# Performance work log

Measured on AMD Instinct MI355X. Metric: run time of the kernel, lower is better.

Reference implementation:

```python
import jax, jax.numpy as jnp
import numpy as np

N, F, H, E, R = 100000, 256, 64, 800000, 7
EPS = 1e-5

def _layernorm(x, g, b):
    mu = jnp.mean(x, axis=-1, keepdims=True)
    var = jnp.mean((x - mu) ** 2, axis=-1, keepdims=True)
    return (x - mu) * jax.lax.rsqrt(var + EPS) * g + b

def setup_inputs() -> dict:
    key = jax.random.key(0)
    ks = jax.random.split(key, 16)
    block_features = jax.random.normal(ks[0], (N, F), dtype=jnp.float32)
    src = jax.random.randint(ks[1], (E,), 0, N).astype(jnp.float32)
    dst = jax.random.randint(ks[2], (E,), 0, N).astype(jnp.float32)
    rel = jax.random.randint(ks[3], (E,), 0, R).astype(jnp.float32)
    w = jax.random.uniform(ks[4], (E,), dtype=jnp.float32)
    typed_edges = jnp.stack([src, dst, rel, w], axis=1)  # [E,4]
    def lin(k, fan_in, fan_out):
        s = 1.0 / np.sqrt(fan_in)
        k1, k2 = jax.random.split(k)
        return (jax.random.uniform(k1, (fan_in, fan_out), jnp.float32, -s, s),
                jax.random.uniform(k2, (fan_out,), jnp.float32, -s, s))
    W1, b1 = lin(ks[5], F, H)
    W2, b2 = lin(ks[6], H, H)
    rel_emb = jax.random.normal(ks[7], (R, H), dtype=jnp.float32)
    Wm1, bm1 = lin(ks[8], 3 * H + 1, H)
    Wm2, bm2 = lin(ks[9], H, H)
    Wg1, bg1 = lin(ks[10], 2 * H, H)
    Wg2, bg2 = lin(ks[11], H, H)
    return dict(block_features=block_features, typed_edges=typed_edges,
                W1=W1, b1=b1, g1=jnp.ones(H), be1=jnp.zeros(H), W2=W2, b2=b2,
                rel_emb=rel_emb, Wm1=Wm1, bm1=bm1, Wm2=Wm2, bm2=bm2,
                gn=jnp.ones(H), bn=jnp.zeros(H), Wg1=Wg1, bg1=bg1, Wg2=Wg2, bg2=bg2)

def reference(block_features, typed_edges, W1, b1, g1, be1, W2, b2, rel_emb,
              Wm1, bm1, Wm2, bm2, gn, bn, Wg1, bg1, Wg2, bg2):
    # node_proj: Linear -> LN -> ReLU -> Linear -> ReLU
    h = jax.nn.relu(_layernorm(block_features @ W1 + b1, g1, be1))
    h = jax.nn.relu(h @ W2 + b2)  # [N,H]
    src = typed_edges[:, 0].astype(jnp.int32)
    dst = typed_edges[:, 1].astype(jnp.int32)
    rel = typed_edges[:, 2].astype(jnp.int32)
    w = typed_edges[:, 3:4]  # [E,1]
    m_in = jnp.concatenate([h[src], h[dst], rel_emb[rel], w], axis=-1)  # [E,3H+1]
    msg = jax.nn.relu(m_in @ Wm1 + bm1) @ Wm2 + bm2  # [E,H]
    agg = jax.ops.segment_sum(msg, dst, num_segments=h.shape[0])  # [N,H]
    nodes = _layernorm(h + agg, gn, bn)
    g = jnp.concatenate([nodes.mean(axis=0), nodes.max(axis=0)], axis=-1)  # [2H]
    return jax.nn.relu(g @ Wg1 + bg1) @ Wg2 + bg2  # [H]
```

## Files before the change

kernel.cpp:

```cpp
#include <hip/hip_runtime.h>

typedef unsigned short u16;
typedef unsigned int   u32;
typedef __attribute__((ext_vector_type(8))) short bf16x8;
typedef __attribute__((ext_vector_type(4))) float f32x4;

#define EPS 1e-5f
#define MFMA(a,b,c) __builtin_amdgcn_mfma_f32_16x16x32_bf16(a,b,c,0,0,0)

constexpr int OB_b1=0, OB_g1=64, OB_be1=128, OB_b2=192, OB_bm1=256, OB_w192=320,
              OB_bm2=384, OB_gn=448, OB_bn=512, OB_bg1=576, OB_bg2=640,
              OB_Wg1=704, OB_Wg2=8896, WB_TOT=12992;
constexpr int FR_Wm1=0;
constexpr int FR_Wm2=12288;
constexpr int FR_rel=16384;
constexpr int FR_W1 =16960;
constexpr int FR_W2 =33344;
constexpr int FR_TOT=37440;

__device__ __forceinline__ float bf2f(u32 u) { return __uint_as_float(u << 16); }
__device__ __forceinline__ u16 f2bf(float f) {
  u32 b = __float_as_uint(f);
  return (u16)((b + 0x7fffu + ((b >> 16) & 1u)) >> 16);
}
__device__ __forceinline__ u32 fkey(float f) {
  u32 b = __float_as_uint(f);
  return (b & 0x80000000u) ? ~b : (b | 0x80000000u);
}

__launch_bounds__(256)
__global__ void k_prep(const float* __restrict__ W1, const float* __restrict__ b1,
                       const float* __restrict__ g1, const float* __restrict__ be1,
                       const float* __restrict__ W2, const float* __restrict__ b2,
                       const float* __restrict__ rel_emb,
                       const float* __restrict__ Wm1, const float* __restrict__ bm1,
                       const float* __restrict__ Wm2, const float* __restrict__ bm2,
                       const float* __restrict__ gn, const float* __restrict__ bn,
                       const float* __restrict__ Wg1, const float* __restrict__ bg1,
                       const float* __restrict__ Wg2, const float* __restrict__ bg2,
                       float* __restrict__ wbuf, u16* __restrict__ frags) {
  int tid = blockIdx.x * 256 + threadIdx.x;
  int nth = gridDim.x * 256;
  for (int i = tid; i < 64; i += nth) {
    wbuf[OB_b1 + i] = b1[i];   wbuf[OB_g1 + i] = g1[i];
    wbuf[OB_be1 + i] = be1[i]; wbuf[OB_b2 + i] = b2[i];
    wbuf[OB_bm1 + i] = bm1[i]; wbuf[OB_w192 + i] = Wm1[192 * 64 + i];
    wbuf[OB_bm2 + i] = bm2[i]; wbuf[OB_gn + i] = gn[i];
    wbuf[OB_bn + i] = bn[i];   wbuf[OB_bg1 + i] = bg1[i];
    wbuf[OB_bg2 + i] = bg2[i];
  }
  for (int i = tid; i < 8192; i += nth) wbuf[OB_Wg1 + i] = Wg1[i];
  for (int i = tid; i < 4096; i += nth) wbuf[OB_Wg2 + i] = Wg2[i];
  for (int idx = tid; idx < 16384; idx += nth) {
    int f = idx >> 9, L = (idx >> 3) & 63, j = idx & 7;
    int k = (f >> 2) * 32 + ((L >> 4) << 3) + j, n = ((f & 3) << 4) + (L & 15);
    frags[FR_W1 + idx] = f2bf(W1[k * 64 + n]);
  }
  for (int idx = tid; idx < 4096; idx += nth) {
    int f = idx >> 9, L = (idx >> 3) & 63, j = idx & 7;
    int k = (f >> 2) * 32 + ((L >> 4) << 3) + j, n = ((f & 3) << 4) + (L & 15);
    frags[FR_W2 + idx] = f2bf(W2[k * 64 + n]);
  }
  for (int idx = tid; idx < 12288; idx += nth) {
    int f = idx >> 9, L = (idx >> 3) & 63, j = idx & 7;
    int k = (f >> 2) * 32 + ((L >> 4) << 3) + j, n = ((f & 3) << 4) + (L & 15);
    frags[FR_Wm1 + idx] = f2bf(Wm1[k * 64 + n]);
  }
  for (int idx = tid; idx < 4096; idx += nth) {
    int f = idx >> 9, L = (idx >> 3) & 63, j = idx & 7;
    int k = (f >> 2) * 32 + ((L >> 4) << 3) + j, n = ((f & 3) << 4) + (L & 15);
    frags[FR_Wm2 + idx] = f2bf(Wm2[k * 64 + n]);
  }
  for (int idx = tid; idx < 576; idx += nth) {
    int r = idx / 80, c = idx % 80;
    frags[FR_rel + idx] = (r < 7 && c < 64) ? f2bf(rel_emb[r * 64 + c]) : (u16)0;
  }
}

__launch_bounds__(256)
__global__ void k_hist(const float* __restrict__ te, int* __restrict__ cnt, int E, int N) {
  int i = blockIdx.x * 256 + threadIdx.x, st = gridDim.x * 256;
  for (int e = i; e < E; e += st) {
    float4 v = *(const float4*)(te + (size_t)e * 4);
    int d = min(max((int)v.y, 0), N - 1);
    atomicAdd(&cnt[d], 1);
  }
}

#define SCH 512
__launch_bounds__(256)
__global__ void k_scan1(const int* __restrict__ cnt, int* __restrict__ bsum, int N) {
  __shared__ int sd[256];
  int b = blockIdx.x, t = threadIdx.x, base = b * SCH;
  int i0 = base + 2 * t, i1 = i0 + 1;
  int a = 0;
  if (i0 < N) a += cnt[i0];
  if (i1 < N) a += cnt[i1];
  sd[t] = a; __syncthreads();
  for (int s = 128; s > 0; s >>= 1) { if (t < s) sd[t] += sd[t + s]; __syncthreads(); }
  if (t == 0) bsum[b] = sd[0];
}

__launch_bounds__(256)
__global__ void k_scan2(const int* __restrict__ bsum, int* __restrict__ bofs,
                        int* __restrict__ ofs, int NBLK, int N) {
  __shared__ int sd[256];
  int t = threadIdx.x;
  int K = (NBLK + 255) / 256;
  int loc = 0;
  for (int k = 0; k < K; k++) { int i = t * K + k; if (i < NBLK) loc += bsum[i]; }
  sd[t] = loc; __syncthreads();
  for (int s = 1; s < 256; s <<= 1) {
    int o = 0; if (t >= s) o = sd[t - s];
    __syncthreads(); sd[t] += o; __syncthreads();
  }
  int excl = sd[t] - loc;
  int run = excl;
  for (int k = 0; k < K; k++) {
    int i = t * K + k;
    if (i < NBLK) { bofs[i] = run; run += bsum[i]; }
  }
  if (t == 255) ofs[N] = sd[255];
}

__launch_bounds__(256)
__global__ void k_scan3(const int* __restrict__ bofs, int* __restrict__ ofs,
                        int* __restrict__ cur, int N) {
  __shared__ int sd[256];
  int b = blockIdx.x, t = threadIdx.x, base = b * SCH;
  int i0 = base + 2 * t, i1 = i0 + 1;
  int a0 = (i0 < N) ? cur[i0] : 0, a1 = (i1 < N) ? cur[i1] : 0;
  int pair = a0 + a1;
  sd[t] = pair; __syncthreads();
  for (int s = 1; s < 256; s <<= 1) {
    int o = 0; if (t >= s) o = sd[t - s];
    __syncthreads(); sd[t] += o; __syncthreads();
  }
  int excl = sd[t] - pair + bofs[b];
  if (i0 < N) { ofs[i0] = excl;      cur[i0] = excl; }
  if (i1 < N) { ofs[i1] = excl + a0; cur[i1] = excl + a0; }
}

__launch_bounds__(256)
__global__ void k_place(const float* __restrict__ te, int* __restrict__ cur,
                        uint4* __restrict__ sorted, int E, int N) {
  int i = blockIdx.x * 256 + threadIdx.x, st = gridDim.x * 256;
  for (int e = i; e < E; e += st) {
    float4 v = *(const float4*)(te + (size_t)e * 4);
    int s = min(max((int)v.x, 0), N - 1);
    int d = min(max((int)v.y, 0), N - 1);
    int r = min(max((int)v.z, 0), 6);
    int pos = atomicAdd(&cur[d], 1);
    uint4 rec; rec.x = (u32)s; rec.y = (u32)d; rec.z = (u32)r; rec.w = __float_as_uint(v.w);
    sorted[pos] = rec;
  }
}

__launch_bounds__(256, 5)
__global__ void k_h(const float* __restrict__ X, const float* __restrict__ wbuf,
                    const u16* __restrict__ frags, u16* __restrict__ hb,
                    float* __restrict__ agg, int N) {
  __shared__ __align__(16) u16 st[4][16 * 72];

  int lane = threadIdx.x & 63, wave = threadIdx.x >> 6;
  int m = lane & 15, quad = lane >> 4, koff = quad * 8, col0 = m;

  int ntiles = (N + 15) / 16;
  int tile = blockIdx.x * 4 + wave;
  if (tile >= ntiles) return;

  float b1v[4], g1v[4], be1v[4], b2v[4];
  #pragma unroll
  for (int nt = 0; nt < 4; nt++) {
    int c = nt * 16 + col0;
    b1v[nt] = wbuf[OB_b1 + c]; g1v[nt] = wbuf[OB_g1 + c];
    be1v[nt] = wbuf[OB_be1 + c]; b2v[nt] = wbuf[OB_b2 + c];
  }

  int n0 = tile * 16;
  int nm = min(n0 + m, N - 1);
  const float* xr = X + (size_t)nm * 256 + koff;
  const u16* fW1 = frags + FR_W1 + lane * 8;
  const u16* fW2 = frags + FR_W2 + lane * 8;

  float4 xv[16];
  #pragma unroll
  for (int ks = 0; ks < 8; ks++) {
    xv[2 * ks]     = *(const float4*)(xr + ks * 32);
    xv[2 * ks + 1] = *(const float4*)(xr + ks * 32 + 4);
  }

  f32x4 acc[4] = {};
  #pragma unroll
  for (int ks = 0; ks < 8; ks++) {
    bf16x8 a;
    a[0] = (short)f2bf(xv[2 * ks].x); a[1] = (short)f2bf(xv[2 * ks].y);
    a[2] = (short)f2bf(xv[2 * ks].z); a[3] = (short)f2bf(xv[2 * ks].w);
    a[4] = (short)f2bf(xv[2 * ks + 1].x); a[5] = (short)f2bf(xv[2 * ks + 1].y);
    a[6] = (short)f2bf(xv[2 * ks + 1].z); a[7] = (short)f2bf(xv[2 * ks + 1].w);
    #pragma unroll
    for (int nt = 0; nt < 4; nt++) {
      bf16x8 b = *(const bf16x8*)(fW1 + (ks * 4 + nt) * 512);
      acc[nt] = MFMA(a, b, acc[nt]);
    }
  }

  float v[4][4];
  #pragma unroll
  for (int nt = 0; nt < 4; nt++)
    #pragma unroll
    for (int r = 0; r < 4; r++) v[nt][r] = acc[nt][r] + b1v[nt];

  #pragma unroll
  for (int r = 0; r < 4; r++) {
    float s = v[0][r] + v[1][r] + v[2][r] + v[3][r];
    #pragma unroll
    for (int mk = 8; mk >= 1; mk >>= 1) s += __shfl_xor(s, mk, 64);
    float mu = s * (1.f / 64.f);
    float q = 0.f;
    #pragma unroll
    for (int nt = 0; nt < 4; nt++) { float d = v[nt][r] - mu; q += d * d; }
    #pragma unroll
    for (int mk = 8; mk >= 1; mk >>= 1) q += __shfl_xor(q, mk, 64);
    float rs = rsqrtf(q * (1.f / 64.f) + EPS);
    #pragma unroll
    for (int nt = 0; nt < 4; nt++) {
      float h1 = fmaxf(fmaf((v[nt][r] - mu) * rs, g1v[nt], be1v[nt]), 0.f);
      st[wave][(quad * 4 + r) * 72 + nt * 16 + col0] = f2bf(h1);
    }
  }
  __builtin_amdgcn_wave_barrier();

  f32x4 acc2[4] = {};
  #pragma unroll
  for (int ks = 0; ks < 2; ks++) {
    bf16x8 a2 = *(const bf16x8*)(st[wave] + m * 72 + ks * 32 + koff);
    #pragma unroll
    for (int nt = 0; nt < 4; nt++) {
      bf16x8 b = *(const bf16x8*)(fW2 + (ks * 4 + nt) * 512);
      acc2[nt] = MFMA(a2, b, acc2[nt]);
    }
  }
  __builtin_amdgcn_wave_barrier();

  #pragma unroll
  for (int nt = 0; nt < 4; nt++)
    #pragma unroll
    for (int r = 0; r < 4; r++) {
      int row = n0 + quad * 4 + r;
      if (row < N) {
        float hv = fmaxf(acc2[nt][r] + b2v[nt], 0.f);
        hb[(size_t)row * 64 + nt * 16 + col0] = f2bf(hv);
        agg[(size_t)row * 64 + nt * 16 + col0] = hv;
      }
    }
}

__launch_bounds__(512, 4)
__global__ void k_edge(const uint4* __restrict__ sorted, const u16* __restrict__ hb,
                       const float* __restrict__ wbuf, const u16* __restrict__ frags,
                       float* __restrict__ agg, int E, int N) {
  __shared__ __align__(16) u16 sWm1[24 * 512];
  __shared__ __align__(16) u16 sWm2[8 * 512];
  __shared__ __align__(16) u16 srel[576];
  __shared__ __align__(16) float st32[8][16 * 68];
  __shared__ int sdst[8][16];

  {
    const uint4* s1 = (const uint4*)(frags + FR_Wm1);
    uint4* d1 = (uint4*)sWm1;
    for (int i = threadIdx.x; i < 1536; i += 512) d1[i] = s1[i];
    const uint4* s2 = (const uint4*)(frags + FR_Wm2);
    uint4* d2 = (uint4*)sWm2;
    for (int i = threadIdx.x; i < 512; i += 512) d2[i] = s2[i];
    const uint4* s3 = (const uint4*)(frags + FR_rel);
    uint4* d3 = (uint4*)srel;
    for (int i = threadIdx.x; i < 72; i += 512) d3[i] = s3[i];
  }
  __syncthreads();

  int lane = threadIdx.x & 63, wave = threadIdx.x >> 6;
  int m = lane & 15, quad = lane >> 4, koff = quad * 8, col0 = m;
  float* st = st32[wave];
  int* dstS = sdst[wave];

  float bm1v[4], w192v[4], bm2v[4];
  #pragma unroll
  for (int nt = 0; nt < 4; nt++) {
    int c = nt * 16 + col0;
    bm1v[nt] = wbuf[OB_bm1 + c];
    w192v[nt] = wbuf[OB_w192 + c];
    bm2v[nt] = wbuf[OB_bm2 + c];
  }

  int ntiles = (E + 15) >> 4;
  int gw = blockIdx.x * 8 + wave, nw = gridDim.x * 8;
  int per = (ntiles + nw - 1) / nw;
  int tile = gw * per, tend = min(tile + per, ntiles);

  int cd = -1; float cv = 0.f;

  for (; tile < tend; tile++) {
    int e0 = tile * 16;
    int src = 0, dstv = 0, rel = 0; float w = 0.f;
    if (lane < 16) {
      int e = e0 + lane;
      uint4 rc = sorted[min(e, E - 1)];
      src = (int)rc.x; dstv = (int)rc.y; rel = (int)rc.z; w = __uint_as_float(rc.w);
      dstS[lane] = (e < E) ? dstv : -1;
    }
    int sm = __shfl(src, m, 64), dm = __shfl(dstv, m, 64), rm = __shfl(rel, m, 64);

    const u16* hs = hb + (size_t)sm * 64;
    const u16* hd = hb + (size_t)dm * 64;
    bf16x8 af[6];
    af[0] = *(const bf16x8*)(hs + koff);
    af[1] = *(const bf16x8*)(hs + 32 + koff);
    af[2] = *(const bf16x8*)(hd + koff);
    af[3] = *(const bf16x8*)(hd + 32 + koff);
    af[4] = *(const bf16x8*)(srel + rm * 80 + koff);
    af[5] = *(const bf16x8*)(srel + rm * 80 + 32 + koff);

    f32x4 acc[4] = {};
    #pragma unroll
    for (int ks = 0; ks < 6; ks++)
      #pragma unroll
      for (int nt = 0; nt < 4; nt++) {
        bf16x8 b = *(const bf16x8*)(sWm1 + (ks * 4 + nt) * 512 + lane * 8);
        acc[nt] = MFMA(af[ks], b, acc[nt]);
      }

    float wrow[4];
    #pragma unroll
    for (int r = 0; r < 4; r++) wrow[r] = __shfl(w, quad * 4 + r, 64);
    #pragma unroll
    for (int nt = 0; nt < 4; nt++)
      #pragma unroll
      for (int r = 0; r < 4; r++) {
        float v = fmaf(wrow[r], w192v[nt], acc[nt][r] + bm1v[nt]);
        st[(quad * 4 + r) * 68 + nt * 16 + col0] = fmaxf(v, 0.f);
      }
    __builtin_amdgcn_wave_barrier();

    f32x4 acc2[4] = {};
    #pragma unroll
    for (int ks = 0; ks < 2; ks++) {
      float4 p0 = *(const float4*)(st + m * 68 + ks * 32 + koff);
      float4 p1 = *(const float4*)(st + m * 68 + ks * 32 + koff + 4);
      bf16x8 a2;
      a2[0] = (short)f2bf(p0.x); a2[1] = (short)f2bf(p0.y);
      a2[2] = (short)f2bf(p0.z); a2[3] = (short)f2bf(p0.w);
      a2[4] = (short)f2bf(p1.x); a2[5] = (short)f2bf(p1.y);
      a2[6] = (short)f2bf(p1.z); a2[7] = (short)f2bf(p1.w);
      #pragma unroll
      for (int nt = 0; nt < 4; nt++) {
        bf16x8 b = *(const bf16x8*)(sWm2 + (ks * 4 + nt) * 512 + lane * 8);
        acc2[nt] = MFMA(a2, b, acc2[nt]);
      }
    }
    __builtin_amdgcn_wave_barrier();

    #pragma unroll
    for (int nt = 0; nt < 4; nt++)
      #pragma unroll
      for (int r = 0; r < 4; r++)
        st[(quad * 4 + r) * 68 + nt * 16 + col0] = acc2[nt][r] + bm2v[nt];
    __builtin_amdgcn_wave_barrier();

    #pragma unroll
    for (int r = 0; r < 16; r++) {
      int d = dstS[r];
      float v = st[r * 68 + lane];
      if (d != cd) {
        if (cd >= 0) atomicAdd(agg + (size_t)cd * 64 + lane, cv);
        cd = d; cv = 0.f;
      }
      if (d >= 0) cv += v;
    }
    __builtin_amdgcn_wave_barrier();
  }
  if (cd >= 0) atomicAdd(agg + (size_t)cd * 64 + lane, cv);
}

__launch_bounds__(256)
__global__ void k_nodes(const float* __restrict__ agg, const float* __restrict__ wbuf,
                        float* __restrict__ gsum, u32* __restrict__ gmax, int N) {
  int lane = threadIdx.x & 63, wave = threadIdx.x >> 6;
  int r4 = lane >> 4, c4 = (lane & 15) * 4;
  float4 gnv = *(const float4*)(wbuf + OB_gn + c4);
  float4 bnv = *(const float4*)(wbuf + OB_bn + c4);
  int wid = blockIdx.x * 4 + wave, nw = gridDim.x * 4;
  float sj[4] = {0.f, 0.f, 0.f, 0.f};
  float mj[4] = {-3.0e38f, -3.0e38f, -3.0e38f, -3.0e38f};
  for (int base = wid * 4; base < N; base += nw * 4) {
    int row = base + r4;
    bool ok = row < N;
    float4 av = ok ? *(const float4*)(agg + (size_t)row * 64 + c4)
                   : make_float4(0.f, 0.f, 0.f, 0.f);
    float s = av.x + av.y + av.z + av.w;
    #pragma unroll
    for (int mk = 8; mk >= 1; mk >>= 1) s += __shfl_xor(s, mk, 64);
    float mu = s * (1.f / 64.f);
    float d0 = av.x - mu, d1 = av.y - mu, d2 = av.z - mu, d3 = av.w - mu;
    float q = d0 * d0 + d1 * d1 + d2 * d2 + d3 * d3;
    #pragma unroll
    for (int mk = 8; mk >= 1; mk >>= 1) q += __shfl_xor(q, mk, 64);
    float rs = rsqrtf(q * (1.f / 64.f) + EPS);
    if (ok) {
      float t0 = fmaf(d0 * rs, gnv.x, bnv.x);
      float t1 = fmaf(d1 * rs, gnv.y, bnv.y);
      float t2 = fmaf(d2 * rs, gnv.z, bnv.z);
      float t3 = fmaf(d3 * rs, gnv.w, bnv.w);
      sj[0] += t0; mj[0] = fmaxf(mj[0], t0);
      sj[1] += t1; mj[1] = fmaxf(mj[1], t1);
      sj[2] += t2; mj[2] = fmaxf(mj[2], t2);
      sj[3] += t3; mj[3] = fmaxf(mj[3], t3);
    }
  }
  #pragma unroll
  for (int j = 0; j < 4; j++) {
    sj[j] += __shfl_xor(sj[j], 16, 64);
    sj[j] += __shfl_xor(sj[j], 32, 64);
    mj[j] = fmaxf(mj[j], __shfl_xor(mj[j], 16, 64));
    mj[j] = fmaxf(mj[j], __shfl_xor(mj[j], 32, 64));
  }
  __shared__ float bs[4][64], bm[4][64];
  if (lane < 16) {
    #pragma unroll
    for (int j = 0; j < 4; j++) { bs[wave][c4 + j] = sj[j]; bm[wave][c4 + j] = mj[j]; }
  }
  __syncthreads();
  if (threadIdx.x < 64) {
    int c = threadIdx.x;
    float ts = bs[0][c] + bs[1][c] + bs[2][c] + bs[3][c];
    float tm = fmaxf(fmaxf(bm[0][c], bm[1][c]), fmaxf(bm[2][c], bm[3][c]));
    atomicAdd(gsum + c, ts);
    atomicMax(gmax + c, fkey(tm));
  }
}

__launch_bounds__(128)
__global__ void k_final(const float* __restrict__ wbuf, const float* __restrict__ gsum,
                        const u32* __restrict__ gmax, float* __restrict__ out, int N) {
  __shared__ float g[128];
  __shared__ float y1[64];
  int t = threadIdx.x;
  if (t < 64) {
    g[t] = gsum[t] / (float)N;
  } else {
    u32 k = gmax[t - 64];
    u32 b = (k & 0x80000000u) ? (k & 0x7fffffffu) : ~k;
    g[t] = __uint_as_float(b);
  }
  __syncthreads();
  if (t < 64) {
    float a = wbuf[OB_bg1 + t];
    for (int i = 0; i < 128; i++) a = fmaf(g[i], wbuf[OB_Wg1 + i * 64 + t], a);
    y1[t] = fmaxf(a, 0.f);
  }
  __syncthreads();
  if (t < 64) {
    float a = wbuf[OB_bg2 + t];
    for (int k = 0; k < 64; k++) a = fmaf(y1[k], wbuf[OB_Wg2 + k * 64 + t], a);
    out[t] = a;
  }
}

extern "C" void kernel_launch(void* const* d_in, const int* in_sizes, int n_in,
                              void* d_out, int out_size, void* d_ws, size_t ws_size,
                              hipStream_t stream) {
  const int N = in_sizes[0] / 256;
  const int E = in_sizes[1] / 4;
  const int NBLK = (N + SCH - 1) / SCH;
  const int NT_H = (N + 15) / 16;

  char* ws = (char*)d_ws;
  size_t p = 0;
  auto rup = [](size_t x) { return (x + 255) & ~(size_t)255; };
  uint4* sorted = (uint4*)(ws + p); p += rup((size_t)E * 16);
  float* agg    = (float*)(ws + p); p += rup((size_t)N * 64 * 4);
  u16*   hb     = (u16*)(ws + p);   p += rup((size_t)N * 128);
  int*   ofs    = (int*)(ws + p);   p += rup((size_t)(N + 1) * 4);
  int*   cur    = (int*)(ws + p);   p += rup((size_t)N * 4);
  int*   bsum   = (int*)(ws + p);   p += rup((size_t)(NBLK + 1) * 4);
  int*   bofs   = (int*)(ws + p);   p += rup((size_t)(NBLK + 1) * 4);
  float* gsum   = (float*)(ws + p); p += 256;
  u32*   gmax   = (u32*)(ws + p);   p += 256;
  float* wbuf   = (float*)(ws + p); p += rup((size_t)WB_TOT * 4);
  u16*   frags  = (u16*)(ws + p);   p += rup((size_t)FR_TOT * 2);

  const float* X  = (const float*)d_in[0];
  const float* te = (const float*)d_in[1];

  hipLaunchKernelGGL(k_prep, dim3(64), dim3(256), 0, stream,
                     (const float*)d_in[2], (const float*)d_in[3], (const float*)d_in[4],
                     (const float*)d_in[5], (const float*)d_in[6], (const float*)d_in[7],
                     (const float*)d_in[8], (const float*)d_in[9], (const float*)d_in[10],
                     (const float*)d_in[11], (const float*)d_in[12], (const float*)d_in[13],
                     (const float*)d_in[14], (const float*)d_in[15], (const float*)d_in[16],
                     (const float*)d_in[17], (const float*)d_in[18], wbuf, frags);
  hipMemsetAsync(cur, 0, (size_t)N * 4, stream);
  hipMemsetAsync(gsum, 0, 512, stream);

  hipLaunchKernelGGL(k_hist, dim3(1024), dim3(256), 0, stream, te, cur, E, N);
  hipLaunchKernelGGL(k_scan1, dim3(NBLK), dim3(256), 0, stream, cur, bsum, N);
  hipLaunchKernelGGL(k_scan2, dim3(1), dim3(256), 0, stream, bsum, bofs, ofs, NBLK, N);
  hipLaunchKernelGGL(k_scan3, dim3(NBLK), dim3(256), 0, stream, bofs, ofs, cur, N);
  hipLaunchKernelGGL(k_place, dim3(1024), dim3(256), 0, stream, te, cur, sorted, E, N);

  hipLaunchKernelGGL(k_h, dim3((NT_H + 3) / 4), dim3(256), 0, stream, X, wbuf, frags, hb, agg, N);
  hipLaunchKernelGGL(k_edge, dim3(512), dim3(512), 0, stream, sorted, hb, wbuf, frags, agg, E, N);
  hipLaunchKernelGGL(k_nodes, dim3(2048), dim3(256), 0, stream, agg, wbuf, gsum, gmax, N);
  hipLaunchKernelGGL(k_final, dim3(1), dim3(128), 0, stream, wbuf, gsum, gmax, (float*)d_out, N);
}
```

Baseline: 418.6 us.

## Restructure node projection as persistent double-buffered LDS pipeline; fuse histogram into prep

The node-projection kernel becomes persistent over a fixed grid. Each block double-buffers 16-row tiles of X into LDS with global_load_lds and an XOR swizzle, and each wave owns one 16-column slice with W1/W2 fragments kept in registers. LayerNorm statistics are now combined across waves through shared memory using a sum and sum-of-squares form, which adds block barriers and a slightly different variance formula. Separately, the edge histogram and the gsum/gmax zeroing are folded into the prep kernel, removing one launch and one memset.

```diff
diff --git a/kernel.cpp b/kernel.cpp
--- a/kernel.cpp
+++ b/kernel.cpp
@@ -26,6 +26,12 @@
 __device__ __forceinline__ u32 fkey(float f) {
   u32 b = __float_as_uint(f);
   return (b & 0x80000000u) ? ~b : (b | 0x80000000u);
+}
+
+__device__ __forceinline__ void gld_lds16(const void* g, void* l) {
+  __builtin_amdgcn_global_load_lds(
+      (const __attribute__((address_space(1))) void*)g,
+      (__attribute__((address_space(3))) void*)l, 16, 0, 0);
 }
 
 __launch_bounds__(256)
@@ -38,7 +44,9 @@
                        const float* __restrict__ gn, const float* __restrict__ bn,
                        const float* __restrict__ Wg1, const float* __restrict__ bg1,
                        const float* __restrict__ Wg2, const float* __restrict__ bg2,
-                       float* __restrict__ wbuf, u16* __restrict__ frags) {
+                       float* __restrict__ wbuf, u16* __restrict__ frags,
+                       const float* __restrict__ te, int* __restrict__ cnt,
+                       float* __restrict__ gsum, u32* __restrict__ gmax, int E, int N) {
   int tid = blockIdx.x * 256 + threadIdx.x;
   int nth = gridDim.x * 256;
   for (int i = tid; i < 64; i += nth) {
@@ -48,6 +56,7 @@
     wbuf[OB_bm2 + i] = bm2[i]; wbuf[OB_gn + i] = gn[i];
     wbuf[OB_bn + i] = bn[i];   wbuf[OB_bg1 + i] = bg1[i];
     wbuf[OB_bg2 + i] = bg2[i];
+    gsum[i] = 0.f; gmax[i] = 0u;
   }
   for (int i = tid; i < 8192; i += nth) wbuf[OB_Wg1 + i] = Wg1[i];
   for (int i = tid; i < 4096; i += nth) wbuf[OB_Wg2 + i] = Wg2[i];
@@ -75,12 +84,7 @@
     int r = idx / 80, c = idx % 80;
     frags[FR_rel + idx] = (r < 7 && c < 64) ? f2bf(rel_emb[r * 64 + c]) : (u16)0;
   }
-}
-
-__launch_bounds__(256)
-__global__ void k_hist(const float* __restrict__ te, int* __restrict__ cnt, int E, int N) {
-  int i = blockIdx.x * 256 + threadIdx.x, st = gridDim.x * 256;
-  for (int e = i; e < E; e += st) {
+  for (int e = tid; e < E; e += nth) {
     float4 v = *(const float4*)(te + (size_t)e * 4);
     int d = min(max((int)v.y, 0), N - 1);
     atomicAdd(&cnt[d], 1);
@@ -156,104 +160,112 @@
   }
 }
 
-__launch_bounds__(256, 5)
+__launch_bounds__(256, 4)
 __global__ void k_h(const float* __restrict__ X, const float* __restrict__ wbuf,
                     const u16* __restrict__ frags, u16* __restrict__ hb,
                     float* __restrict__ agg, int N) {
-  __shared__ __align__(16) u16 st[4][16 * 72];
+  __shared__ __align__(16) float xb[2][16 * 256];
+  __shared__ __align__(16) u16 st[16 * 72];
+  __shared__ float sred[2][16][4];
 
   int lane = threadIdx.x & 63, wave = threadIdx.x >> 6;
-  int m = lane & 15, quad = lane >> 4, koff = quad * 8, col0 = m;
+  int m = lane & 15, quad = lane >> 4;
+  int col = wave * 16 + m;
+
+  bf16x8 bw1[8], bw2[2];
+  #pragma unroll
+  for (int ks = 0; ks < 8; ks++)
+    bw1[ks] = *(const bf16x8*)(frags + FR_W1 + ((ks * 4 + wave) * 64 + lane) * 8);
+  #pragma unroll
+  for (int ks = 0; ks < 2; ks++)
+    bw2[ks] = *(const bf16x8*)(frags + FR_W2 + ((ks * 4 + wave) * 64 + lane) * 8);
+
+  float b1v = wbuf[OB_b1 + col], g1v = wbuf[OB_g1 + col];
+  float be1v = wbuf[OB_be1 + col], b2v = wbuf[OB_b2 + col];
 
   int ntiles = (N + 15) / 16;
-  int tile = blockIdx.x * 4 + wave;
-  if (tile >= ntiles) return;
-
-  float b1v[4], g1v[4], be1v[4], b2v[4];
-  #pragma unroll
-  for (int nt = 0; nt < 4; nt++) {
-    int c = nt * 16 + col0;
-    b1v[nt] = wbuf[OB_b1 + c]; g1v[nt] = wbuf[OB_g1 + c];
-    be1v[nt] = wbuf[OB_be1 + c]; b2v[nt] = wbuf[OB_b2 + c];
-  }
-
-  int n0 = tile * 16;
-  int nm = min(n0 + m, N - 1);
-  const float* xr = X + (size_t)nm * 256 + koff;
-  const u16* fW1 = frags + FR_W1 + lane * 8;
-  const u16* fW2 = frags + FR_W2 + lane * 8;
-
-  float4 xv[16];
-  #pragma unroll
-  for (int ks = 0; ks < 8; ks++) {
-    xv[2 * ks]     = *(const float4*)(xr + ks * 32);
-    xv[2 * ks + 1] = *(const float4*)(xr + ks * 32 + 4);
-  }
-
-  f32x4 acc[4] = {};
-  #pragma unroll
-  for (int ks = 0; ks < 8; ks++) {
-    bf16x8 a;
-    a[0] = (short)f2bf(xv[2 * ks].x); a[1] = (short)f2bf(xv[2 * ks].y);
-    a[2] = (short)f2bf(xv[2 * ks].z); a[3] = (short)f2bf(xv[2 * ks].w);
-    a[4] = (short)f2bf(xv[2 * ks + 1].x); a[5] = (short)f2bf(xv[2 * ks + 1].y);
-    a[6] = (short)f2bf(xv[2 * ks + 1].z); a[7] = (short)f2bf(xv[2 * ks + 1].w);
-    #pragma unroll
-    for (int nt = 0; nt < 4; nt++) {
-      bf16x8 b = *(const bf16x8*)(fW1 + (ks * 4 + nt) * 512);
-      acc[nt] = MFMA(a, b, acc[nt]);
-    }
-  }
-
-  float v[4][4];
-  #pragma unroll
-  for (int nt = 0; nt < 4; nt++)
-    #pragma unroll
-    for (int r = 0; r < 4; r++) v[nt][r] = acc[nt][r] + b1v[nt];
-
-  #pragma unroll
-  for (int r = 0; r < 4; r++) {
-    float s = v[0][r] + v[1][r] + v[2][r] + v[3][r];
-    #pragma unroll
-    for (int mk = 8; mk >= 1; mk >>= 1) s += __shfl_xor(s, mk, 64);
-    float mu = s * (1.f / 64.f);
-    float q = 0.f;
-    #pragma unroll
-    for (int nt = 0; nt < 4; nt++) { float d = v[nt][r] - mu; q += d * d; }
-    #pragma unroll
-    for (int mk = 8; mk >= 1; mk >>= 1) q += __shfl_xor(q, mk, 64);
-    float rs = rsqrtf(q * (1.f / 64.f) + EPS);
-    #pragma unroll
-    for (int nt = 0; nt < 4; nt++) {
-      float h1 = fmaxf(fmaf((v[nt][r] - mu) * rs, g1v[nt], be1v[nt]), 0.f);
-      st[wave][(quad * 4 + r) * 72 + nt * 16 + col0] = f2bf(h1);
-    }
-  }
-  __builtin_amdgcn_wave_barrier();
-
-  f32x4 acc2[4] = {};
-  #pragma unroll
-  for (int ks = 0; ks < 2; ks++) {
-    bf16x8 a2 = *(const bf16x8*)(st[wave] + m * 72 + ks * 32 + koff);
-    #pragma unroll
-    for (int nt = 0; nt < 4; nt++) {
-      bf16x8 b = *(const bf16x8*)(fW2 + (ks * 4 + nt) * 512);
-      acc2[nt] = MFMA(a2, b, acc2[nt]);
-    }
-  }
-  __builtin_amdgcn_wave_barrier();
-
-  #pragma unroll
-  for (int nt = 0; nt < 4; nt++)
+  int xorm = (m & 7) << 4;
+
+  auto stage = [&](int t, int buf) {
+    int n0s = t * 16;
+    #pragma unroll
+    for (int i = 0; i < 4; i++) {
+      int r = wave * 4 + i;
+      int nr = min(n0s + r, N - 1);
+      const char* src = (const char*)(X + (size_t)nr * 256);
+      int soff = (lane * 16) ^ ((r & 7) << 4);
+      gld_lds16(src + soff, (char*)&xb[buf][0] + r * 1024);
+    }
+  };
+
+  int cur = 0;
+  if (blockIdx.x < ntiles) stage(blockIdx.x, 0);
+
+  for (int t = blockIdx.x; t < ntiles; t += gridDim.x) {
+    __syncthreads();
+    if (t + (int)gridDim.x < ntiles) stage(t + gridDim.x, cur ^ 1);
+
+    int n0 = t * 16;
+    const char* xp = (const char*)&xb[cur][0];
+
+    f32x4 acc = {};
+    #pragma unroll
+    for (int ks = 0; ks < 8; ks++) {
+      int base = m * 1024 + ks * 128 + quad * 32;
+      float4 u0 = *(const float4*)(xp + (base ^ xorm));
+      float4 u1 = *(const float4*)(xp + ((base + 16) ^ xorm));
+      bf16x8 a;
+      a[0] = (short)f2bf(u0.x); a[1] = (short)f2bf(u0.y);
+      a[2] = (short)f2bf(u0.z); a[3] = (short)f2bf(u0.w);
+      a[4] = (short)f2bf(u1.x); a[5] = (short)f2bf(u1.y);
+      a[6] = (short)f2bf(u1.z); a[7] = (short)f2bf(u1.w);
+      acc = MFMA(a, bw1[ks], acc);
+    }
+
+    float vv[4];
+    #pragma unroll
+    for (int r = 0; r < 4; r++) vv[r] = acc[r] + b1v;
+    #pragma unroll
+    for (int r = 0; r < 4; r++) {
+      float s = vv[r], q = vv[r] * vv[r];
+      #pragma unroll
+      for (int mk = 8; mk >= 1; mk >>= 1) {
+        s += __shfl_xor(s, mk, 64);
+        q += __shfl_xor(q, mk, 64);
+      }
+      if (m == 0) { sred[0][quad * 4 + r][wave] = s; sred[1][quad * 4 + r][wave] = q; }
+    }
+    __syncthreads();
+    #pragma unroll
+    for (int r = 0; r < 4; r++) {
+      int row = quad * 4 + r;
+      float4 S = *(const float4*)&sred[0][row][0];
+      float4 Q = *(const float4*)&sred[1][row][0];
+      float mu = (S.x + S.y + S.z + S.w) * (1.f / 64.f);
+      float vq = (Q.x + Q.y + Q.z + Q.w) * (1.f / 64.f) - mu * mu;
+      float rs = rsqrtf(fmaxf(vq, 0.f) + EPS);
+      float h1 = fmaxf(fmaf((vv[r] - mu) * rs, g1v, be1v), 0.f);
+      st[row * 72 + col] = f2bf(h1);
+    }
+    __syncthreads();
+
+    f32x4 acc2 = {};
+    #pragma unroll
+    for (int ks = 0; ks < 2; ks++) {
+      bf16x8 a2 = *(const bf16x8*)(st + m * 72 + ks * 32 + quad * 8);
+      acc2 = MFMA(a2, bw2[ks], acc2);
+    }
     #pragma unroll
     for (int r = 0; r < 4; r++) {
       int row = n0 + quad * 4 + r;
       if (row < N) {
-        float hv = fmaxf(acc2[nt][r] + b2v[nt], 0.f);
-        hb[(size_t)row * 64 + nt * 16 + col0] = f2bf(hv);
-        agg[(size_t)row * 64 + nt * 16 + col0] = hv;
+        float hv = fmaxf(acc2[r] + b2v, 0.f);
+        hb[(size_t)row * 64 + col] = f2bf(hv);
+        agg[(size_t)row * 64 + col] = hv;
       }
     }
+    cur ^= 1;
+  }
 }
 
 __launch_bounds__(512, 4)
@@ -472,7 +484,6 @@
   const int N = in_sizes[0] / 256;
   const int E = in_sizes[1] / 4;
   const int NBLK = (N + SCH - 1) / SCH;
-  const int NT_H = (N + 15) / 16;
 
   char* ws = (char*)d_ws;
   size_t p = 0;
@@ -492,23 +503,22 @@
   const float* X  = (const float*)d_in[0];
   const float* te = (const float*)d_in[1];
 
-  hipLaunchKernelGGL(k_prep, dim3(64), dim3(256), 0, stream,
+  hipMemsetAsync(cur, 0, (size_t)N * 4, stream);
+  hipLaunchKernelGGL(k_prep, dim3(1024), dim3(256), 0, stream,
                      (const float*)d_in[2], (const float*)d_in[3], (const float*)d_in[4],
                      (const float*)d_in[5], (const float*)d_in[6], (const float*)d_in[7],
                      (const float*)d_in[8], (const float*)d_in[9], (const float*)d_in[10],
                      (const float*)d_in[11], (const float*)d_in[12], (const float*)d_in[13],
                      (const float*)d_in[14], (const float*)d_in[15], (const float*)d_in[16],
-                     (const float*)d_in[17], (const float*)d_in[18], wbuf, frags);
-  hipMemsetAsync(cur, 0, (size_t)N * 4, stream);
-  hipMemsetAsync(gsum, 0, 512, stream);
-
-  hipLaunchKernelGGL(k_hist, dim3(1024), dim3(256), 0, stream, te, cur, E, N);
+                     (const float*)d_in[17], (const float*)d_in[18], wbuf, frags,
+                     te, cur, gsum, gmax, E, N);
+
   hipLaunchKernelGGL(k_scan1, dim3(NBLK), dim3(256), 0, stream, cur, bsum, N);
   hipLaunchKernelGGL(k_scan2, dim3(1), dim3(256), 0, stream, bsum, bofs, ofs, NBLK, N);
   hipLaunchKernelGGL(k_scan3, dim3(NBLK), dim3(256), 0, stream, bofs, ofs, cur, N);
   hipLaunchKernelGGL(k_place, dim3(1024), dim3(256), 0, stream, te, cur, sorted, E, N);
 
-  hipLaunchKernelGGL(k_h, dim3((NT_H + 3) / 4), dim3(256), 0, stream, X, wbuf, frags, hb, agg, N);
+  hipLaunchKernelGGL(k_h, dim3(1024), dim3(256), 0, stream, X, wbuf, frags, hb, agg, N);
   hipLaunchKernelGGL(k_edge, dim3(512), dim3(512), 0, stream, sorted, hb, wbuf, frags, agg, E, N);
   hipLaunchKernelGGL(k_nodes, dim3(2048), dim3(256), 0, stream, agg, wbuf, gsum, gmax, N);
   hipLaunchKernelGGL(k_final, dim3(1), dim3(128), 0, stream, wbuf, gsum, gmax, (float*)d_out, N);
```

Result: faster. 400.6 us (-4.3%).
